# Optimization experiments

Measured on AMD Instinct MI355X. Metric: run time of the kernel, lower is better.

## Reference

```python
import jax, jax.numpy as jnp
import numpy as np

EMB = 1024

def setup_inputs() -> dict:
    key = jax.random.key(0)
    ks = jax.random.split(key, 7)
    s = 1.0 / np.sqrt(EMB)
    x = jax.random.normal(ks[0], (4, 2048, EMB), dtype=jnp.float32)
    Wk = jax.random.normal(ks[1], (EMB, EMB), dtype=jnp.float32) * s
    bk = jnp.zeros((EMB,), dtype=jnp.float32)
    Wq = jax.random.normal(ks[2], (EMB, EMB), dtype=jnp.float32) * s
    bq = jnp.zeros((EMB,), dtype=jnp.float32)
    Wv = jax.random.normal(ks[3], (EMB, EMB), dtype=jnp.float32) * s
    bv = jnp.zeros((EMB,), dtype=jnp.float32)
    return {"x": x, "Wk": Wk, "bk": bk, "Wq": Wq, "bq": bq, "Wv": Wv, "bv": bv}

def reference(x, Wk, bk, Wq, bq, Wv, bv):
    # Linear layers: x @ W.T + b (torch nn.Linear convention)
    k = jnp.einsum('bse,fe->bsf', x, Wk) + bk
    q = jnp.einsum('bse,fe->bsf', x, Wq) + bq
    v = jnp.einsum('bse,fe->bsf', x, Wv) + bv
    E = x.shape[-1]
    # NOTE: original computes k @ q^T (not q @ k^T) — reproduce faithfully.
    sim = jnp.einsum('bsd,btd->bst', k, q) / jnp.sqrt(jnp.float32(E))
    S = x.shape[1]
    causal = jnp.tril(jnp.ones((S, S), dtype=bool))  # [S,S]
    sim = jnp.where(causal, sim, -jnp.inf)
    attn = jax.nn.softmax(sim, axis=-1)
    return jnp.einsum('bst,btd->bsd', attn, v)
```

## Files before the change

### kernel.cpp

```cpp
#include <hip/hip_runtime.h>
#include <cstdint>


typedef __attribute__((ext_vector_type(8))) _Float16 f16x8;
typedef __attribute__((ext_vector_type(4))) float f32x4;

__device__ __forceinline__ unsigned short f2h(float x) {
  return __builtin_bit_cast(unsigned short, (_Float16)x);
}

__device__ __forceinline__ void lds_dma16(const void* g, void* l) {
  auto gp = reinterpret_cast<const __attribute__((address_space(1))) void*>(
      reinterpret_cast<uintptr_t>(g));
  auto lp = reinterpret_cast<__attribute__((address_space(3))) void*>(
      reinterpret_cast<uintptr_t>(l));
  __builtin_amdgcn_global_load_lds(gp, lp, 16, 0, 0);
}

__device__ __forceinline__ void gemm128(const unsigned short* __restrict__ Ag,
                                        const unsigned short* __restrict__ Bg,
                                        int lda, int ldb, int nk,
                                        unsigned short* As, unsigned short* Bs,
                                        f32x4 acc[4][4]) {
  const int tid = threadIdx.x;
  const int lane = tid & 63, wave = tid >> 6;
  const int wm = wave >> 1, wn = wave & 1;
  const int sr = lane >> 2;
  const int scb = (((lane & 3) ^ ((lane >> 3) & 3)) * 8);
  const int rr = lane & 15, qq = lane >> 4;
  const int slot = ((qq ^ ((rr >> 1) & 3)) * 8);

#pragma unroll
  for (int i = 0; i < 4; ++i)
#pragma unroll
    for (int j = 0; j < 4; ++j) {
      f32x4 z = {0.f, 0.f, 0.f, 0.f};
      acc[i][j] = z;
    }

#pragma unroll
  for (int c = 0; c < 2; ++c) {
    int chunk = wave * 2 + c;
    int row = chunk * 16 + sr;
    lds_dma16(Ag + (size_t)row * lda + scb, As + chunk * 512);
    lds_dma16(Bg + (size_t)row * ldb + scb, Bs + chunk * 512);
  }

  int buf = 0;
  for (int k0 = 0; k0 < nk; k0 += 32) {
    __syncthreads();
    const int kn = k0 + 32;
    if (kn < nk) {
      unsigned short* An = As + (buf ^ 1) * 4096;
      unsigned short* Bn = Bs + (buf ^ 1) * 4096;
#pragma unroll
      for (int c = 0; c < 2; ++c) {
        int chunk = wave * 2 + c;
        int row = chunk * 16 + sr;
        lds_dma16(Ag + (size_t)row * lda + kn + scb, An + chunk * 512);
        lds_dma16(Bg + (size_t)row * ldb + kn + scb, Bn + chunk * 512);
      }
    }

    f16x8 af[4], bf[4];
    const unsigned short* Ar = As + buf * 4096 + (wm * 64 + rr) * 32 + slot;
    const unsigned short* Br = Bs + buf * 4096 + (wn * 64 + rr) * 32 + slot;
#pragma unroll
    for (int i = 0; i < 4; ++i) af[i] = *(const f16x8*)(Ar + i * 512);
#pragma unroll
    for (int j = 0; j < 4; ++j) bf[j] = *(const f16x8*)(Br + j * 512);
#pragma unroll
    for (int i = 0; i < 4; ++i)
#pragma unroll
      for (int j = 0; j < 4; ++j)
        acc[i][j] = __builtin_amdgcn_mfma_f32_16x16x32_f16(af[i], bf[j],
                                                           acc[i][j], 0, 0, 0);
    buf ^= 1;
  }
}

__device__ __forceinline__ void gemm128_k64(
    const unsigned short* __restrict__ Ag, const unsigned short* __restrict__ Bg,
    int lda, int ldb, int nk, unsigned short* As, unsigned short* Bs,
    f32x4 acc[4][4]) {
  const int tid = threadIdx.x;
  const int lane = tid & 63, wave = tid >> 6;
  const int wm = wave >> 1, wn = wave & 1;
  const int sr = lane >> 3;
  const int scb = ((lane & 7) ^ sr) * 8;
  const int rr = lane & 15, qq = lane >> 4;
  const int slot0 = ((qq) ^ (rr & 7)) * 8;
  const int slot1 = ((4 + qq) ^ (rr & 7)) * 8;

#pragma unroll
  for (int i = 0; i < 4; ++i)
#pragma unroll
    for (int j = 0; j < 4; ++j) {
      f32x4 z = {0.f, 0.f, 0.f, 0.f};
      acc[i][j] = z;
    }

#pragma unroll
  for (int c = 0; c < 4; ++c) {
    int chunk = wave * 4 + c;
    int row = chunk * 8 + sr;
    lds_dma16(Ag + (size_t)row * lda + scb, As + chunk * 512);
    lds_dma16(Bg + (size_t)row * ldb + scb, Bs + chunk * 512);
  }

  int buf = 0;
  for (int k0 = 0; k0 < nk; k0 += 64) {
    __syncthreads();
    const int kn = k0 + 64;
    if (kn < nk) {
      unsigned short* An = As + (buf ^ 1) * 8192;
      unsigned short* Bn = Bs + (buf ^ 1) * 8192;
#pragma unroll
      for (int c = 0; c < 4; ++c) {
        int chunk = wave * 4 + c;
        int row = chunk * 8 + sr;
        lds_dma16(Ag + (size_t)row * lda + kn + scb, An + chunk * 512);
        lds_dma16(Bg + (size_t)row * ldb + kn + scb, Bn + chunk * 512);
      }
    }

    const unsigned short* Ar = As + buf * 8192 + (wm * 64 + rr) * 64;
    const unsigned short* Br = Bs + buf * 8192 + (wn * 64 + rr) * 64;
    {
      f16x8 af[4], bf[4];
#pragma unroll
      for (int i = 0; i < 4; ++i) af[i] = *(const f16x8*)(Ar + i * 1024 + slot0);
#pragma unroll
      for (int j = 0; j < 4; ++j) bf[j] = *(const f16x8*)(Br + j * 1024 + slot0);
#pragma unroll
      for (int i = 0; i < 4; ++i)
#pragma unroll
        for (int j = 0; j < 4; ++j)
          acc[i][j] = __builtin_amdgcn_mfma_f32_16x16x32_f16(af[i], bf[j],
                                                             acc[i][j], 0, 0, 0);
    }
    {
      f16x8 af[4], bf[4];
#pragma unroll
      for (int i = 0; i < 4; ++i) af[i] = *(const f16x8*)(Ar + i * 1024 + slot1);
#pragma unroll
      for (int j = 0; j < 4; ++j) bf[j] = *(const f16x8*)(Br + j * 1024 + slot1);
#pragma unroll
      for (int i = 0; i < 4; ++i)
#pragma unroll
        for (int j = 0; j < 4; ++j)
          acc[i][j] = __builtin_amdgcn_mfma_f32_16x16x32_f16(af[i], bf[j],
                                                             acc[i][j], 0, 0, 0);
    }
    buf ^= 1;
  }
}

__global__ void cvt_kernel(const float* __restrict__ x,
                           const float* __restrict__ w0,
                           const float* __restrict__ w1,
                           const float* __restrict__ w2,
                           unsigned short* __restrict__ dst,
                           float* __restrict__ rsum) {
  int i = blockIdx.x * 256 + threadIdx.x;
  if (i >= 2883584) {
    int z2 = i - 2883584;
    float4 z = {0.f, 0.f, 0.f, 0.f};
    ((float4*)rsum)[z2] = z;
    return;
  }
  const float* s;
  size_t si;
  if (i < 2097152) {
    s = x; si = i;
  } else {
    int j = i - 2097152;
    int z = j >> 18;
    s = (z == 0) ? w0 : ((z == 1) ? w1 : w2);
    si = j & 262143;
  }
  float4 f = ((const float4*)s)[si];
  ushort4 u;
  u.x = f2h(f.x); u.y = f2h(f.y); u.z = f2h(f.z); u.w = f2h(f.w);
  ((ushort4*)dst)[i] = u;
}

__global__ __launch_bounds__(256) void qkv_gemm_kernel(
    const unsigned short* __restrict__ xh, const unsigned short* __restrict__ wh,
    const float* __restrict__ bk, const float* __restrict__ bq,
    const float* __restrict__ bv, unsigned short* __restrict__ kh,
    unsigned short* __restrict__ qh, unsigned short* __restrict__ vT) {
  __shared__ unsigned short As[2 * 128 * 32], Bs[2 * 128 * 32];
  const int tn = blockIdx.x & 7, z = blockIdx.x >> 3;
  const unsigned short* W = wh + (size_t)z * 1048576;
  const int tm = blockIdx.y;

  const unsigned short* Ag = (z == 2) ? (W + (size_t)tn * 128 * 1024)
                                      : (xh + (size_t)tm * 128 * 1024);
  const unsigned short* Bg = (z == 2) ? (xh + (size_t)tm * 128 * 1024)
                                      : (W + (size_t)tn * 128 * 1024);

  f32x4 acc[4][4];
  gemm128(Ag, Bg, 1024, 1024, 1024, As, Bs, acc);

  const int lane = threadIdx.x & 63, wave = threadIdx.x >> 6;
  const int wm = wave >> 1, wn = wave & 1, rr = lane & 15, qq = lane >> 4;

  if (z == 2) {
#pragma unroll
    for (int i = 0; i < 4; ++i) {
      int d0 = tn * 128 + wm * 64 + i * 16 + qq * 4;
      float4 bi = *(const float4*)(bv + d0);
      float bir[4] = {bi.x, bi.y, bi.z, bi.w};
#pragma unroll
      for (int reg = 0; reg < 4; ++reg) {
        int d = d0 + reg;
#pragma unroll
        for (int j = 0; j < 4; ++j) {
          int tg = tm * 128 + wn * 64 + j * 16 + rr;
          int bb = tg >> 11, tt = tg & 2047;
          vT[((size_t)(bb * 1024 + d)) * 2048 + tt] =
              f2h(acc[i][j][reg] + bir[reg]);
        }
      }
    }
  } else {
    const float* bias = (z == 0) ? bk : bq;
    unsigned short* dst = (z == 0) ? kh : qh;
    float bj[4];
#pragma unroll
    for (int j = 0; j < 4; ++j)
      bj[j] = bias[tn * 128 + wn * 64 + j * 16 + rr];
#pragma unroll
    for (int i = 0; i < 4; ++i)
#pragma unroll
      for (int reg = 0; reg < 4; ++reg) {
        int gm = tm * 128 + wm * 64 + i * 16 + qq * 4 + reg;
#pragma unroll
        for (int j = 0; j < 4; ++j) {
          int gc = tn * 128 + wn * 64 + j * 16 + rr;
          dst[(size_t)gm * 1024 + gc] = f2h(acc[i][j][reg] + bj[j]);
        }
      }
  }
}

__global__ __launch_bounds__(256) void scores_kernel(
    const unsigned short* __restrict__ kh, const unsigned short* __restrict__ qh,
    unsigned short* __restrict__ P, float* __restrict__ rsum) {
  const int b = blockIdx.y;
  int idx = blockIdx.x;
  int ts = (int)((sqrtf(8.0f * idx + 1.0f) - 1.0f) * 0.5f);
  while ((ts + 1) * (ts + 2) / 2 <= idx) ++ts;
  while (ts * (ts + 1) / 2 > idx) --ts;
  const int tt = idx - ts * (ts + 1) / 2;
  __shared__ unsigned short As[2 * 128 * 64], Bs[2 * 128 * 64];

  f32x4 acc[4][4];
  gemm128_k64(kh + ((size_t)(b * 2048 + ts * 128)) * 1024,
              qh + ((size_t)(b * 2048 + tt * 128)) * 1024,
              1024, 1024, 1024, As, Bs, acc);

  const int lane = threadIdx.x & 63, wave = threadIdx.x >> 6;
  const int wm = wave >> 1, wn = wave & 1, rr = lane & 15, qq = lane >> 4;
  unsigned short* Pb = P + (size_t)b * 2048 * 2048;
  float* rs = rsum + b * 2048;
#pragma unroll
  for (int i = 0; i < 4; ++i)
#pragma unroll
    for (int reg = 0; reg < 4; ++reg) {
      int srow = ts * 128 + wm * 64 + i * 16 + qq * 4 + reg;
      float p = 0.f;
#pragma unroll
      for (int j = 0; j < 4; ++j) {
        int tcol = tt * 128 + wn * 64 + j * 16 + rr;
        float e = (tcol <= srow) ? __expf(acc[i][j][reg] * 0.03125f - 4.0f)
                                 : 0.0f;
        Pb[(size_t)srow * 2048 + tcol] = f2h(e);
        p += e;
      }
#pragma unroll
      for (int off = 1; off < 16; off <<= 1) p += __shfl_xor(p, off);
      if (rr == 0) atomicAdd(rs + srow, p);
    }
}

__global__ __launch_bounds__(256) void pv_gemm_kernel(
    const unsigned short* __restrict__ P, const unsigned short* __restrict__ vT,
    const float* __restrict__ rsum, float* __restrict__ out) {
  const int td = blockIdx.x, ts = 15 - blockIdx.y, b = blockIdx.z;
  __shared__ unsigned short As[2 * 128 * 64], Bs[2 * 128 * 64];

  f32x4 acc[4][4];
  gemm128_k64(P + ((size_t)(b * 2048 + ts * 128)) * 2048,
              vT + ((size_t)(b * 1024 + td * 128)) * 2048,
              2048, 2048, (ts + 1) * 128, As, Bs, acc);

  const int lane = threadIdx.x & 63, wave = threadIdx.x >> 6;
  const int wm = wave >> 1, wn = wave & 1, rr = lane & 15, qq = lane >> 4;
#pragma unroll
  for (int i = 0; i < 4; ++i) {
    int s0 = ts * 128 + wm * 64 + i * 16 + qq * 4;
    float4 r4 = *(const float4*)(rsum + b * 2048 + s0);
    float rv[4] = {__builtin_amdgcn_rcpf(r4.x), __builtin_amdgcn_rcpf(r4.y),
                   __builtin_amdgcn_rcpf(r4.z), __builtin_amdgcn_rcpf(r4.w)};
#pragma unroll
    for (int reg = 0; reg < 4; ++reg) {
      int srow = s0 + reg;
#pragma unroll
      for (int j = 0; j < 4; ++j) {
        int dcol = td * 128 + wn * 64 + j * 16 + rr;
        out[((size_t)(b * 2048 + srow)) * 1024 + dcol] =
            acc[i][j][reg] * rv[reg];
      }
    }
  }
}

extern "C" void kernel_launch(void* const* d_in, const int* in_sizes, int n_in,
                              void* d_out, int out_size, void* d_ws,
                              size_t ws_size, hipStream_t stream) {
  const float* x  = (const float*)d_in[0];
  const float* Wk = (const float*)d_in[1];
  const float* bk = (const float*)d_in[2];
  const float* Wq = (const float*)d_in[3];
  const float* bq = (const float*)d_in[4];
  const float* Wv = (const float*)d_in[5];
  const float* bv = (const float*)d_in[6];
  float* out = (float*)d_out;

  char* ws = (char*)d_ws;
  const size_t MB = 1ull << 20;
  unsigned short* xh = (unsigned short*)(ws + 0);
  unsigned short* wh = (unsigned short*)(ws + 16 * MB);
  unsigned short* P  = (unsigned short*)(ws + 0);
  unsigned short* kh = (unsigned short*)(ws + 38 * MB);
  unsigned short* qh = (unsigned short*)(ws + 54 * MB);
  unsigned short* vT = (unsigned short*)(ws + 70 * MB);
  float* rsum = (float*)(ws + 86 * MB);

  cvt_kernel<<<11272, 256, 0, stream>>>(x, Wk, Wq, Wv, xh, rsum);
  qkv_gemm_kernel<<<dim3(24, 64), 256, 0, stream>>>(xh, wh, bk, bq, bv,
                                                    kh, qh, vT);
  scores_kernel<<<dim3(136, 4), 256, 0, stream>>>(kh, qh, P, rsum);
  pv_gemm_kernel<<<dim3(8, 16, 4), 256, 0, stream>>>(P, vT, rsum, out);
}
```

Baseline: 239.7 us.

## Replace QKV projection GEMM with 256x256-tile, 8-wave pipelined kernel

The 128x128 QKV GEMM with K-step 32 is replaced by a 256x256 output tile per 512-thread block, using K-step 64 stages split into half-tiles. Staging is interleaved with the eight quadrant sub-iterations and controlled by explicit waitcnt, barriers and setprio, and the block-to-job mapping is remapped for L2 locality. The larger tile reuses each staged operand across more MMAs and cuts global traffic. In exchange it uses more LDS and registers per block, and the hand-tuned counter waits risk subtle races.

```diff
diff --git a/kernel.cpp b/kernel.cpp
--- a/kernel.cpp
+++ b/kernel.cpp
@@ -17,66 +17,113 @@
   __builtin_amdgcn_global_load_lds(gp, lp, 16, 0, 0);
 }
 
-__device__ __forceinline__ void gemm128(const unsigned short* __restrict__ Ag,
-                                        const unsigned short* __restrict__ Bg,
-                                        int lda, int ldb, int nk,
-                                        unsigned short* As, unsigned short* Bs,
-                                        f32x4 acc[4][4]) {
+__device__ __forceinline__ void stage_half(const unsigned short* __restrict__ G,
+                                           int ld, unsigned short* lds,
+                                           int tid) {
+  const int r = tid >> 3;
+  const int c = ((tid & 7) ^ (r & 7)) * 8;
+  lds_dma16(G + (size_t)r * ld + c, lds + tid * 8);
+  lds_dma16(G + (size_t)(r + 64) * ld + c, lds + 4096 + tid * 8);
+}
+
+__device__ __forceinline__ void g256_iter(
+    const unsigned short* __restrict__ Ag, const unsigned short* __restrict__ Bg,
+    int lda, int ldb, unsigned short* As, unsigned short* Bs,
+    f32x4 (&acc)[2][2][2][4], int k0, bool last) {
   const int tid = threadIdx.x;
   const int lane = tid & 63, wave = tid >> 6;
-  const int wm = wave >> 1, wn = wave & 1;
-  const int sr = lane >> 2;
-  const int scb = (((lane & 3) ^ ((lane >> 3) & 3)) * 8);
+  const int qwm = wave >> 1, qwn = wave & 1;
   const int rr = lane & 15, qq = lane >> 4;
-  const int slot = ((qq ^ ((rr >> 1) & 3)) * 8);
-
-#pragma unroll
-  for (int i = 0; i < 4; ++i)
-#pragma unroll
-    for (int j = 0; j < 4; ++j) {
-      f32x4 z = {0.f, 0.f, 0.f, 0.f};
-      acc[i][j] = z;
-    }
-
-#pragma unroll
-  for (int c = 0; c < 2; ++c) {
-    int chunk = wave * 2 + c;
-    int row = chunk * 16 + sr;
-    lds_dma16(Ag + (size_t)row * lda + scb, As + chunk * 512);
-    lds_dma16(Bg + (size_t)row * ldb + scb, Bs + chunk * 512);
-  }
-
-  int buf = 0;
-  for (int k0 = 0; k0 < nk; k0 += 32) {
-    __syncthreads();
-    const int kn = k0 + 32;
-    if (kn < nk) {
-      unsigned short* An = As + (buf ^ 1) * 4096;
-      unsigned short* Bn = Bs + (buf ^ 1) * 4096;
-#pragma unroll
-      for (int c = 0; c < 2; ++c) {
-        int chunk = wave * 2 + c;
-        int row = chunk * 16 + sr;
-        lds_dma16(Ag + (size_t)row * lda + kn + scb, An + chunk * 512);
-        lds_dma16(Bg + (size_t)row * ldb + kn + scb, Bn + chunk * 512);
+  const int arow = (qwm * 32 + rr) * 64;
+  const int brow = (qwn * 64 + rr) * 64;
+  const int s7 = rr & 7;
+  const int soff0 = (qq ^ s7) * 8;
+  const int soff1 = ((4 + qq) ^ s7) * 8;
+
+#pragma unroll
+  for (int p = 0; p < 8; ++p) {
+    const int buf = p >> 2, qm = (p >> 1) & 1, qn = p & 1;
+    const unsigned short* Ar = As + buf * 16384 + qm * 8192 + arow;
+    const unsigned short* Br = Bs + buf * 16384 + qn * 8192 + brow;
+    f16x8 af[2][2], bf[4][2];
+#pragma unroll
+    for (int fi = 0; fi < 2; ++fi) {
+      af[fi][0] = *(const f16x8*)(Ar + fi * 1024 + soff0);
+      af[fi][1] = *(const f16x8*)(Ar + fi * 1024 + soff1);
+    }
+#pragma unroll
+    for (int fj = 0; fj < 4; ++fj) {
+      bf[fj][0] = *(const f16x8*)(Br + fj * 1024 + soff0);
+      bf[fj][1] = *(const f16x8*)(Br + fj * 1024 + soff1);
+    }
+
+    if (p == 0) {
+      stage_half(Ag + (size_t)128 * lda + (k0 + 64), lda, As + 24576, tid);
+    } else if (p == 1) {
+      stage_half(Bg + (size_t)128 * ldb + (k0 + 64), ldb, Bs + 24576, tid);
+    } else if (!last) {
+      if (p == 2)      stage_half(Ag + (k0 + 128), lda, As, tid);
+      else if (p == 3) stage_half(Bg + (k0 + 128), ldb, Bs, tid);
+      else if (p == 4) stage_half(Ag + (size_t)128 * lda + (k0 + 128), lda, As + 8192, tid);
+      else if (p == 5) stage_half(Bg + (size_t)128 * ldb + (k0 + 128), ldb, Bs + 8192, tid);
+      else if (p == 6) stage_half(Ag + (k0 + 192), lda, As + 16384, tid);
+      else             stage_half(Bg + (k0 + 192), ldb, Bs + 16384, tid);
+    }
+
+    asm volatile("s_waitcnt lgkmcnt(8)" ::: "memory");
+    __builtin_amdgcn_s_barrier();
+    asm volatile("s_waitcnt lgkmcnt(0)" ::: "memory");
+    __builtin_amdgcn_sched_barrier(0);
+    __builtin_amdgcn_s_setprio(1);
+#pragma unroll
+    for (int h = 0; h < 2; ++h)
+#pragma unroll
+      for (int fi = 0; fi < 2; ++fi)
+#pragma unroll
+        for (int fj = 0; fj < 4; ++fj)
+          acc[qm][qn][fi][fj] = __builtin_amdgcn_mfma_f32_16x16x32_f16(
+              af[fi][h], bf[fj][h], acc[qm][qn][fi][fj], 0, 0, 0);
+    __builtin_amdgcn_s_setprio(0);
+    if (p == 3) {
+      if (last) asm volatile("s_waitcnt vmcnt(0)" ::: "memory");
+      else      asm volatile("s_waitcnt vmcnt(4)" ::: "memory");
+    } else if (p == 7 && !last) {
+      asm volatile("s_waitcnt vmcnt(4)" ::: "memory");
+    }
+    __builtin_amdgcn_s_barrier();
+  }
+}
+
+__device__ __forceinline__ void gemm256(
+    const unsigned short* __restrict__ Ag, const unsigned short* __restrict__ Bg,
+    int lda, int ldb, int nk, unsigned short* As, unsigned short* Bs,
+    f32x4 (&acc)[2][2][2][4]) {
+  const int tid = threadIdx.x;
+#pragma unroll
+  for (int a = 0; a < 2; ++a)
+#pragma unroll
+    for (int b = 0; b < 2; ++b)
+#pragma unroll
+      for (int c = 0; c < 2; ++c)
+#pragma unroll
+      for (int d = 0; d < 4; ++d) {
+        f32x4 z = {0.f, 0.f, 0.f, 0.f};
+        acc[a][b][c][d] = z;
       }
-    }
-
-    f16x8 af[4], bf[4];
-    const unsigned short* Ar = As + buf * 4096 + (wm * 64 + rr) * 32 + slot;
-    const unsigned short* Br = Bs + buf * 4096 + (wn * 64 + rr) * 32 + slot;
-#pragma unroll
-    for (int i = 0; i < 4; ++i) af[i] = *(const f16x8*)(Ar + i * 512);
-#pragma unroll
-    for (int j = 0; j < 4; ++j) bf[j] = *(const f16x8*)(Br + j * 512);
-#pragma unroll
-    for (int i = 0; i < 4; ++i)
-#pragma unroll
-      for (int j = 0; j < 4; ++j)
-        acc[i][j] = __builtin_amdgcn_mfma_f32_16x16x32_f16(af[i], bf[j],
-                                                           acc[i][j], 0, 0, 0);
-    buf ^= 1;
-  }
+
+  stage_half(Ag, lda, As, tid);
+  stage_half(Ag + (size_t)128 * lda, lda, As + 8192, tid);
+  stage_half(Bg, ldb, Bs, tid);
+  stage_half(Bg + (size_t)128 * ldb, ldb, Bs + 8192, tid);
+  stage_half(Ag + 64, lda, As + 16384, tid);
+  stage_half(Bg + 64, ldb, Bs + 16384, tid);
+  asm volatile("s_waitcnt vmcnt(4)" ::: "memory");
+  __builtin_amdgcn_s_barrier();
+
+  const int NIT = nk >> 7;
+  for (int it = 0; it < NIT - 1; ++it)
+    g256_iter(Ag, Bg, lda, ldb, As, Bs, acc, it << 7, false);
+  g256_iter(Ag, Bg, lda, ldb, As, Bs, acc, (NIT - 1) << 7, true);
 }
 
 __device__ __forceinline__ void gemm128_k64(
@@ -185,61 +232,84 @@
   ((ushort4*)dst)[i] = u;
 }
 
-__global__ __launch_bounds__(256) void qkv_gemm_kernel(
+__global__ __launch_bounds__(512, 2) void qkv256_kernel(
     const unsigned short* __restrict__ xh, const unsigned short* __restrict__ wh,
     const float* __restrict__ bk, const float* __restrict__ bq,
     const float* __restrict__ bv, unsigned short* __restrict__ kh,
     unsigned short* __restrict__ qh, unsigned short* __restrict__ vT) {
-  __shared__ unsigned short As[2 * 128 * 32], Bs[2 * 128 * 32];
-  const int tn = blockIdx.x & 7, z = blockIdx.x >> 3;
-  const unsigned short* W = wh + (size_t)z * 1048576;
-  const int tm = blockIdx.y;
-
-  const unsigned short* Ag = (z == 2) ? (W + (size_t)tn * 128 * 1024)
-                                      : (xh + (size_t)tm * 128 * 1024);
-  const unsigned short* Bg = (z == 2) ? (xh + (size_t)tm * 128 * 1024)
-                                      : (W + (size_t)tn * 128 * 1024);
-
-  f32x4 acc[4][4];
-  gemm128(Ag, Bg, 1024, 1024, 1024, As, Bs, acc);
-
-  const int lane = threadIdx.x & 63, wave = threadIdx.x >> 6;
-  const int wm = wave >> 1, wn = wave & 1, rr = lane & 15, qq = lane >> 4;
-
-  if (z == 2) {
-#pragma unroll
-    for (int i = 0; i < 4; ++i) {
-      int d0 = tn * 128 + wm * 64 + i * 16 + qq * 4;
-      float4 bi = *(const float4*)(bv + d0);
-      float bir[4] = {bi.x, bi.y, bi.z, bi.w};
-#pragma unroll
-      for (int reg = 0; reg < 4; ++reg) {
-        int d = d0 + reg;
-#pragma unroll
-        for (int j = 0; j < 4; ++j) {
-          int tg = tm * 128 + wn * 64 + j * 16 + rr;
-          int bb = tg >> 11, tt = tg & 2047;
-          vT[((size_t)(bb * 1024 + d)) * 2048 + tt] =
-              f2h(acc[i][j][reg] + bir[reg]);
+  __shared__ unsigned short As[32768], Bs[32768];
+  const int job = (blockIdx.x & 7) * 48 + (blockIdx.x >> 3);
+
+  const unsigned short* Ag;
+  const unsigned short* Bg;
+  if (job < 256) {
+    const int tm = job >> 3, tn = job & 7;
+    Ag = xh + (size_t)tm * 256 * 1024;
+    Bg = wh + (size_t)tn * 256 * 1024;
+  } else {
+    const int j = job - 256;
+    const int dt = j >> 5, tt = j & 31;
+    Ag = wh + 2097152 + (size_t)dt * 256 * 1024;
+    Bg = xh + (size_t)tt * 256 * 1024;
+  }
+
+  f32x4 acc[2][2][2][4];
+  gemm256(Ag, Bg, 1024, 1024, 1024, As, Bs, acc);
+
+  const int tid = threadIdx.x;
+  const int lane = tid & 63, wave = tid >> 6;
+  const int qwm = wave >> 1, qwn = wave & 1, rr = lane & 15, qq = lane >> 4;
+
+  if (job < 256) {
+    const int tm = job >> 3, tn = job & 7;
+    const bool isq = tn >= 4;
+    unsigned short* dst = isq ? qh : kh;
+    const float* bias = isq ? bq : bk;
+    const int nbase = (tn & 3) * 256;
+    float bj[2][4];
+#pragma unroll
+    for (int qn = 0; qn < 2; ++qn)
+#pragma unroll
+      for (int fj = 0; fj < 4; ++fj)
+        bj[qn][fj] = bias[nbase + qn * 128 + qwn * 64 + fj * 16 + rr];
+#pragma unroll
+    for (int qm = 0; qm < 2; ++qm)
+#pragma unroll
+      for (int fi = 0; fi < 2; ++fi)
+#pragma unroll
+        for (int reg = 0; reg < 4; ++reg) {
+          const int m = tm * 256 + qm * 128 + qwm * 32 + fi * 16 + qq * 4 + reg;
+#pragma unroll
+          for (int qn = 0; qn < 2; ++qn)
+#pragma unroll
+            for (int fj = 0; fj < 4; ++fj) {
+              const int n = nbase + qn * 128 + qwn * 64 + fj * 16 + rr;
+              dst[(size_t)m * 1024 + n] =
+                  f2h(acc[qm][qn][fi][fj][reg] + bj[qn][fj]);
+            }
         }
-      }
-    }
   } else {
-    const float* bias = (z == 0) ? bk : bq;
-    unsigned short* dst = (z == 0) ? kh : qh;
-    float bj[4];
-#pragma unroll
-    for (int j = 0; j < 4; ++j)
-      bj[j] = bias[tn * 128 + wn * 64 + j * 16 + rr];
-#pragma unroll
-    for (int i = 0; i < 4; ++i)
-#pragma unroll
-      for (int reg = 0; reg < 4; ++reg) {
-        int gm = tm * 128 + wm * 64 + i * 16 + qq * 4 + reg;
-#pragma unroll
-        for (int j = 0; j < 4; ++j) {
-          int gc = tn * 128 + wn * 64 + j * 16 + rr;
-          dst[(size_t)gm * 1024 + gc] = f2h(acc[i][j][reg] + bj[j]);
+    const int j = job - 256;
+    const int dt = j >> 5, tt = j & 31;
+#pragma unroll
+    for (int qm = 0; qm < 2; ++qm)
+#pragma unroll
+      for (int fi = 0; fi < 2; ++fi) {
+        const int d0 = dt * 256 + qm * 128 + qwm * 32 + fi * 16 + qq * 4;
+        const float4 b4 = *(const float4*)(bv + d0);
+        const float bir[4] = {b4.x, b4.y, b4.z, b4.w};
+#pragma unroll
+        for (int reg = 0; reg < 4; ++reg) {
+          const int d = d0 + reg;
+#pragma unroll
+          for (int qn = 0; qn < 2; ++qn)
+#pragma unroll
+            for (int fj = 0; fj < 4; ++fj) {
+              const int tg = tt * 256 + qn * 128 + qwn * 64 + fj * 16 + rr;
+              const int bb = tg >> 11, t = tg & 2047;
+              vT[((size_t)(bb * 1024 + d)) * 2048 + t] =
+                  f2h(acc[qm][qn][fi][fj][reg] + bir[reg]);
+            }
         }
       }
   }
@@ -340,8 +410,7 @@
   float* rsum = (float*)(ws + 86 * MB);
 
   cvt_kernel<<<11272, 256, 0, stream>>>(x, Wk, Wq, Wv, xh, rsum);
-  qkv_gemm_kernel<<<dim3(24, 64), 256, 0, stream>>>(xh, wh, bk, bq, bv,
-                                                    kh, qh, vT);
+  qkv256_kernel<<<384, 512, 0, stream>>>(xh, wh, bk, bq, bv, kh, qh, vT);
   scores_kernel<<<dim3(136, 4), 256, 0, stream>>>(kh, qh, P, rsum);
   pv_gemm_kernel<<<dim3(8, 16, 4), 256, 0, stream>>>(P, vT, rsum, out);
 }
```

Result: slower. 244.7 us (+2.1%).

## Use atomic work-queue tile scheduling for scores and PV kernels

Applied to the files above, without the earlier changes.

The scores and PV GEMM kernels now run a fixed grid of 512 blocks that pull tile indices from global atomic counters, instead of mapping one block per tile. The counters are reset in the conversion kernel. PV tiles are dispatched in descending causal-length order across all batches, so the longest K-loops start first. This aims to cut tail imbalance on triangular work, at the cost of an extra atomic and a block-wide barrier per tile.

```diff
diff --git a/kernel.cpp b/kernel.cpp
--- a/kernel.cpp
+++ b/kernel.cpp
@@ -79,6 +79,7 @@
   }
 }
 
+
 __device__ __forceinline__ void gemm128_k64(
     const unsigned short* __restrict__ Ag, const unsigned short* __restrict__ Bg,
     int lda, int ldb, int nk, unsigned short* As, unsigned short* Bs,
@@ -161,12 +162,13 @@
                            const float* __restrict__ w1,
                            const float* __restrict__ w2,
                            unsigned short* __restrict__ dst,
-                           float* __restrict__ rsum) {
+                           float* __restrict__ rsum, int* __restrict__ cnt) {
   int i = blockIdx.x * 256 + threadIdx.x;
   if (i >= 2883584) {
     int z2 = i - 2883584;
     float4 z = {0.f, 0.f, 0.f, 0.f};
     ((float4*)rsum)[z2] = z;
+    if (z2 == 0) { cnt[0] = 0; cnt[1] = 0; }
     return;
   }
   const float* s;
@@ -247,71 +249,93 @@
 
 __global__ __launch_bounds__(256) void scores_kernel(
     const unsigned short* __restrict__ kh, const unsigned short* __restrict__ qh,
-    unsigned short* __restrict__ P, float* __restrict__ rsum) {
-  const int b = blockIdx.y;
-  int idx = blockIdx.x;
-  int ts = (int)((sqrtf(8.0f * idx + 1.0f) - 1.0f) * 0.5f);
-  while ((ts + 1) * (ts + 2) / 2 <= idx) ++ts;
-  while (ts * (ts + 1) / 2 > idx) --ts;
-  const int tt = idx - ts * (ts + 1) / 2;
+    unsigned short* __restrict__ P, float* __restrict__ rsum,
+    int* __restrict__ cnt) {
   __shared__ unsigned short As[2 * 128 * 64], Bs[2 * 128 * 64];
-
-  f32x4 acc[4][4];
-  gemm128_k64(kh + ((size_t)(b * 2048 + ts * 128)) * 1024,
-              qh + ((size_t)(b * 2048 + tt * 128)) * 1024,
-              1024, 1024, 1024, As, Bs, acc);
-
-  const int lane = threadIdx.x & 63, wave = threadIdx.x >> 6;
-  const int wm = wave >> 1, wn = wave & 1, rr = lane & 15, qq = lane >> 4;
-  unsigned short* Pb = P + (size_t)b * 2048 * 2048;
-  float* rs = rsum + b * 2048;
-#pragma unroll
-  for (int i = 0; i < 4; ++i)
-#pragma unroll
-    for (int reg = 0; reg < 4; ++reg) {
-      int srow = ts * 128 + wm * 64 + i * 16 + qq * 4 + reg;
-      float p = 0.f;
-#pragma unroll
-      for (int j = 0; j < 4; ++j) {
-        int tcol = tt * 128 + wn * 64 + j * 16 + rr;
-        float e = (tcol <= srow) ? __expf(acc[i][j][reg] * 0.03125f - 4.0f)
-                                 : 0.0f;
-        Pb[(size_t)srow * 2048 + tcol] = f2h(e);
-        p += e;
-      }
-#pragma unroll
-      for (int off = 1; off < 16; off <<= 1) p += __shfl_xor(p, off);
-      if (rr == 0) atomicAdd(rs + srow, p);
-    }
+  __shared__ int js;
+  const int tid = threadIdx.x;
+
+  for (;;) {
+    if (tid == 0) js = atomicAdd(cnt, 1);
+    __syncthreads();
+    const int j = js;
+    if (j >= 544) return;
+
+    const int b = j / 136;
+    int idx = j - b * 136;
+    int ts = (int)((sqrtf(8.0f * idx + 1.0f) - 1.0f) * 0.5f);
+    while ((ts + 1) * (ts + 2) / 2 <= idx) ++ts;
+    while (ts * (ts + 1) / 2 > idx) --ts;
+    const int tt = idx - ts * (ts + 1) / 2;
+
+    f32x4 acc[4][4];
+    gemm128_k64(kh + ((size_t)(b * 2048 + ts * 128)) * 1024,
+                qh + ((size_t)(b * 2048 + tt * 128)) * 1024,
+                1024, 1024, 1024, As, Bs, acc);
+
+    const int lane = tid & 63, wave = tid >> 6;
+    const int wm = wave >> 1, wn = wave & 1, rr = lane & 15, qq = lane >> 4;
+    unsigned short* Pb = P + (size_t)b * 2048 * 2048;
+    float* rs = rsum + b * 2048;
+#pragma unroll
+    for (int i = 0; i < 4; ++i)
+#pragma unroll
+      for (int reg = 0; reg < 4; ++reg) {
+        int srow = ts * 128 + wm * 64 + i * 16 + qq * 4 + reg;
+        float p = 0.f;
+#pragma unroll
+        for (int jj = 0; jj < 4; ++jj) {
+          int tcol = tt * 128 + wn * 64 + jj * 16 + rr;
+          float e = (tcol <= srow) ? __expf(acc[i][jj][reg] * 0.03125f - 4.0f)
+                                   : 0.0f;
+          Pb[(size_t)srow * 2048 + tcol] = f2h(e);
+          p += e;
+        }
+#pragma unroll
+        for (int off = 1; off < 16; off <<= 1) p += __shfl_xor(p, off);
+        if (rr == 0) atomicAdd(rs + srow, p);
+      }
+  }
 }
 
 __global__ __launch_bounds__(256) void pv_gemm_kernel(
     const unsigned short* __restrict__ P, const unsigned short* __restrict__ vT,
-    const float* __restrict__ rsum, float* __restrict__ out) {
-  const int td = blockIdx.x, ts = 15 - blockIdx.y, b = blockIdx.z;
+    const float* __restrict__ rsum, float* __restrict__ out,
+    int* __restrict__ cnt) {
   __shared__ unsigned short As[2 * 128 * 64], Bs[2 * 128 * 64];
-
-  f32x4 acc[4][4];
-  gemm128_k64(P + ((size_t)(b * 2048 + ts * 128)) * 2048,
-              vT + ((size_t)(b * 1024 + td * 128)) * 2048,
-              2048, 2048, (ts + 1) * 128, As, Bs, acc);
-
-  const int lane = threadIdx.x & 63, wave = threadIdx.x >> 6;
-  const int wm = wave >> 1, wn = wave & 1, rr = lane & 15, qq = lane >> 4;
-#pragma unroll
-  for (int i = 0; i < 4; ++i) {
-    int s0 = ts * 128 + wm * 64 + i * 16 + qq * 4;
-    float4 r4 = *(const float4*)(rsum + b * 2048 + s0);
-    float rv[4] = {__builtin_amdgcn_rcpf(r4.x), __builtin_amdgcn_rcpf(r4.y),
-                   __builtin_amdgcn_rcpf(r4.z), __builtin_amdgcn_rcpf(r4.w)};
-#pragma unroll
-    for (int reg = 0; reg < 4; ++reg) {
-      int srow = s0 + reg;
-#pragma unroll
-      for (int j = 0; j < 4; ++j) {
-        int dcol = td * 128 + wn * 64 + j * 16 + rr;
-        out[((size_t)(b * 2048 + srow)) * 1024 + dcol] =
-            acc[i][j][reg] * rv[reg];
+  __shared__ int js;
+  const int tid = threadIdx.x;
+
+  for (;;) {
+    if (tid == 0) js = atomicAdd(cnt + 1, 1);
+    __syncthreads();
+    const int j = js;
+    if (j >= 512) return;
+
+    const int ts = 15 - (j >> 5), b = (j >> 3) & 3, td = j & 7;
+
+    f32x4 acc[4][4];
+    gemm128_k64(P + ((size_t)(b * 2048 + ts * 128)) * 2048,
+                vT + ((size_t)(b * 1024 + td * 128)) * 2048,
+                2048, 2048, (ts + 1) * 128, As, Bs, acc);
+
+    const int lane = tid & 63, wave = tid >> 6;
+    const int wm = wave >> 1, wn = wave & 1, rr = lane & 15, qq = lane >> 4;
+#pragma unroll
+    for (int i = 0; i < 4; ++i) {
+      int s0 = ts * 128 + wm * 64 + i * 16 + qq * 4;
+      float4 r4 = *(const float4*)(rsum + b * 2048 + s0);
+      float rv[4] = {__builtin_amdgcn_rcpf(r4.x), __builtin_amdgcn_rcpf(r4.y),
+                     __builtin_amdgcn_rcpf(r4.z), __builtin_amdgcn_rcpf(r4.w)};
+#pragma unroll
+      for (int reg = 0; reg < 4; ++reg) {
+        int srow = s0 + reg;
+#pragma unroll
+        for (int jj = 0; jj < 4; ++jj) {
+          int dcol = td * 128 + wn * 64 + jj * 16 + rr;
+          out[((size_t)(b * 2048 + srow)) * 1024 + dcol] =
+              acc[i][jj][reg] * rv[reg];
+        }
       }
     }
   }
@@ -334,14 +358,15 @@
   unsigned short* xh = (unsigned short*)(ws + 0);
   unsigned short* wh = (unsigned short*)(ws + 16 * MB);
   unsigned short* P  = (unsigned short*)(ws + 0);
+  int* cnt = (int*)(ws + 36 * MB);
   unsigned short* kh = (unsigned short*)(ws + 38 * MB);
   unsigned short* qh = (unsigned short*)(ws + 54 * MB);
   unsigned short* vT = (unsigned short*)(ws + 70 * MB);
   float* rsum = (float*)(ws + 86 * MB);
 
-  cvt_kernel<<<11272, 256, 0, stream>>>(x, Wk, Wq, Wv, xh, rsum);
+  cvt_kernel<<<11272, 256, 0, stream>>>(x, Wk, Wq, Wv, xh, rsum, cnt);
   qkv_gemm_kernel<<<dim3(24, 64), 256, 0, stream>>>(xh, wh, bk, bq, bv,
                                                     kh, qh, vT);
-  scores_kernel<<<dim3(136, 4), 256, 0, stream>>>(kh, qh, P, rsum);
-  pv_gemm_kernel<<<dim3(8, 16, 4), 256, 0, stream>>>(P, vT, rsum, out);
-}
+  scores_kernel<<<512, 256, 0, stream>>>(kh, qh, P, rsum, cnt);
+  pv_gemm_kernel<<<512, 256, 0, stream>>>(P, vT, rsum, out, cnt);
+}
```

New measurement: 241.9 us. Within noise of the previous version (+0.9%).

## Split-K PV GEMM with persistent atomic work queue and K32 tiles

Applied to the files above, without the earlier changes.

Drops the K64 GEMM helper and uses the K32 gemm128 for both scores and PV. PV becomes a persistent kernel that pulls jobs from an atomic counter, splits each causal row tile's K range into 512-wide chunks, and accumulates results into out with float atomics. cvt_kernel now zeroes out and the counters. The aim is to balance the triangular PV workload across CUs, at the cost of atomic output traffic, extra zeroing, and nondeterministic summation order.

```diff
diff --git a/kernel.cpp b/kernel.cpp
--- a/kernel.cpp
+++ b/kernel.cpp
@@ -79,94 +79,25 @@
   }
 }
 
-__device__ __forceinline__ void gemm128_k64(
-    const unsigned short* __restrict__ Ag, const unsigned short* __restrict__ Bg,
-    int lda, int ldb, int nk, unsigned short* As, unsigned short* Bs,
-    f32x4 acc[4][4]) {
-  const int tid = threadIdx.x;
-  const int lane = tid & 63, wave = tid >> 6;
-  const int wm = wave >> 1, wn = wave & 1;
-  const int sr = lane >> 3;
-  const int scb = ((lane & 7) ^ sr) * 8;
-  const int rr = lane & 15, qq = lane >> 4;
-  const int slot0 = ((qq) ^ (rr & 7)) * 8;
-  const int slot1 = ((4 + qq) ^ (rr & 7)) * 8;
-
-#pragma unroll
-  for (int i = 0; i < 4; ++i)
-#pragma unroll
-    for (int j = 0; j < 4; ++j) {
-      f32x4 z = {0.f, 0.f, 0.f, 0.f};
-      acc[i][j] = z;
-    }
-
-#pragma unroll
-  for (int c = 0; c < 4; ++c) {
-    int chunk = wave * 4 + c;
-    int row = chunk * 8 + sr;
-    lds_dma16(Ag + (size_t)row * lda + scb, As + chunk * 512);
-    lds_dma16(Bg + (size_t)row * ldb + scb, Bs + chunk * 512);
-  }
-
-  int buf = 0;
-  for (int k0 = 0; k0 < nk; k0 += 64) {
-    __syncthreads();
-    const int kn = k0 + 64;
-    if (kn < nk) {
-      unsigned short* An = As + (buf ^ 1) * 8192;
-      unsigned short* Bn = Bs + (buf ^ 1) * 8192;
-#pragma unroll
-      for (int c = 0; c < 4; ++c) {
-        int chunk = wave * 4 + c;
-        int row = chunk * 8 + sr;
-        lds_dma16(Ag + (size_t)row * lda + kn + scb, An + chunk * 512);
-        lds_dma16(Bg + (size_t)row * ldb + kn + scb, Bn + chunk * 512);
-      }
-    }
-
-    const unsigned short* Ar = As + buf * 8192 + (wm * 64 + rr) * 64;
-    const unsigned short* Br = Bs + buf * 8192 + (wn * 64 + rr) * 64;
-    {
-      f16x8 af[4], bf[4];
-#pragma unroll
-      for (int i = 0; i < 4; ++i) af[i] = *(const f16x8*)(Ar + i * 1024 + slot0);
-#pragma unroll
-      for (int j = 0; j < 4; ++j) bf[j] = *(const f16x8*)(Br + j * 1024 + slot0);
-#pragma unroll
-      for (int i = 0; i < 4; ++i)
-#pragma unroll
-        for (int j = 0; j < 4; ++j)
-          acc[i][j] = __builtin_amdgcn_mfma_f32_16x16x32_f16(af[i], bf[j],
-                                                             acc[i][j], 0, 0, 0);
-    }
-    {
-      f16x8 af[4], bf[4];
-#pragma unroll
-      for (int i = 0; i < 4; ++i) af[i] = *(const f16x8*)(Ar + i * 1024 + slot1);
-#pragma unroll
-      for (int j = 0; j < 4; ++j) bf[j] = *(const f16x8*)(Br + j * 1024 + slot1);
-#pragma unroll
-      for (int i = 0; i < 4; ++i)
-#pragma unroll
-        for (int j = 0; j < 4; ++j)
-          acc[i][j] = __builtin_amdgcn_mfma_f32_16x16x32_f16(af[i], bf[j],
-                                                             acc[i][j], 0, 0, 0);
-    }
-    buf ^= 1;
-  }
-}
-
 __global__ void cvt_kernel(const float* __restrict__ x,
                            const float* __restrict__ w0,
                            const float* __restrict__ w1,
                            const float* __restrict__ w2,
                            unsigned short* __restrict__ dst,
-                           float* __restrict__ rsum) {
+                           float* __restrict__ rsum, int* __restrict__ cnt,
+                           float* __restrict__ out) {
   int i = blockIdx.x * 256 + threadIdx.x;
+  if (i >= 2885632) {
+    int o = i - 2885632;
+    float4 z = {0.f, 0.f, 0.f, 0.f};
+    ((float4*)out)[o] = z;
+    return;
+  }
   if (i >= 2883584) {
     int z2 = i - 2883584;
     float4 z = {0.f, 0.f, 0.f, 0.f};
     ((float4*)rsum)[z2] = z;
+    if (z2 == 0) { cnt[0] = 0; cnt[1] = 0; }
     return;
   }
   const float* s;
@@ -254,12 +185,12 @@
   while ((ts + 1) * (ts + 2) / 2 <= idx) ++ts;
   while (ts * (ts + 1) / 2 > idx) --ts;
   const int tt = idx - ts * (ts + 1) / 2;
-  __shared__ unsigned short As[2 * 128 * 64], Bs[2 * 128 * 64];
+  __shared__ unsigned short As[2 * 128 * 32], Bs[2 * 128 * 32];
 
   f32x4 acc[4][4];
-  gemm128_k64(kh + ((size_t)(b * 2048 + ts * 128)) * 1024,
-              qh + ((size_t)(b * 2048 + tt * 128)) * 1024,
-              1024, 1024, 1024, As, Bs, acc);
+  gemm128(kh + ((size_t)(b * 2048 + ts * 128)) * 1024,
+          qh + ((size_t)(b * 2048 + tt * 128)) * 1024,
+          1024, 1024, 1024, As, Bs, acc);
 
   const int lane = threadIdx.x & 63, wave = threadIdx.x >> 6;
   const int wm = wave >> 1, wn = wave & 1, rr = lane & 15, qq = lane >> 4;
@@ -287,31 +218,57 @@
 
 __global__ __launch_bounds__(256) void pv_gemm_kernel(
     const unsigned short* __restrict__ P, const unsigned short* __restrict__ vT,
-    const float* __restrict__ rsum, float* __restrict__ out) {
-  const int td = blockIdx.x, ts = 15 - blockIdx.y, b = blockIdx.z;
-  __shared__ unsigned short As[2 * 128 * 64], Bs[2 * 128 * 64];
-
-  f32x4 acc[4][4];
-  gemm128_k64(P + ((size_t)(b * 2048 + ts * 128)) * 2048,
-              vT + ((size_t)(b * 1024 + td * 128)) * 2048,
-              2048, 2048, (ts + 1) * 128, As, Bs, acc);
-
-  const int lane = threadIdx.x & 63, wave = threadIdx.x >> 6;
-  const int wm = wave >> 1, wn = wave & 1, rr = lane & 15, qq = lane >> 4;
-#pragma unroll
-  for (int i = 0; i < 4; ++i) {
-    int s0 = ts * 128 + wm * 64 + i * 16 + qq * 4;
-    float4 r4 = *(const float4*)(rsum + b * 2048 + s0);
-    float rv[4] = {__builtin_amdgcn_rcpf(r4.x), __builtin_amdgcn_rcpf(r4.y),
-                   __builtin_amdgcn_rcpf(r4.z), __builtin_amdgcn_rcpf(r4.w)};
-#pragma unroll
-    for (int reg = 0; reg < 4; ++reg) {
-      int srow = s0 + reg;
-#pragma unroll
-      for (int j = 0; j < 4; ++j) {
-        int dcol = td * 128 + wn * 64 + j * 16 + rr;
-        out[((size_t)(b * 2048 + srow)) * 1024 + dcol] =
-            acc[i][j][reg] * rv[reg];
+    const float* __restrict__ rsum, float* __restrict__ out,
+    int* __restrict__ cnt) {
+  __shared__ unsigned short As[2 * 128 * 32], Bs[2 * 128 * 32];
+  __shared__ int js;
+  const int tid = threadIdx.x;
+
+  for (;;) {
+    if (tid == 0) js = atomicAdd(cnt + 1, 1);
+    __syncthreads();
+    const int j = js;
+    if (j >= 1280) return;
+
+    int ts, b, td, kc;
+    if (j < 512) {
+      ts = 15 - (j >> 7); int r = j & 127;
+      b = r >> 5; td = (r >> 2) & 7; kc = r & 3;
+    } else if (j < 896) {
+      int q = j - 512; ts = 11 - q / 96; int r = q % 96;
+      b = r / 24; int r2 = r % 24; td = r2 / 3; kc = r2 % 3;
+    } else if (j < 1152) {
+      int q = j - 896; ts = 7 - (q >> 6); int r = q & 63;
+      b = r >> 4; td = (r >> 1) & 7; kc = r & 1;
+    } else {
+      int q = j - 1152; ts = 3 - (q >> 5); int r = q & 31;
+      b = r >> 3; td = r & 7; kc = 0;
+    }
+    const int kbeg = kc * 512;
+    const int nk = min(512, (ts + 1) * 128 - kbeg);
+
+    f32x4 acc[4][4];
+    gemm128(P + ((size_t)(b * 2048 + ts * 128)) * 2048 + kbeg,
+            vT + ((size_t)(b * 1024 + td * 128)) * 2048 + kbeg,
+            2048, 2048, nk, As, Bs, acc);
+
+    const int lane = tid & 63, wave = tid >> 6;
+    const int wm = wave >> 1, wn = wave & 1, rr = lane & 15, qq = lane >> 4;
+#pragma unroll
+    for (int i = 0; i < 4; ++i) {
+      int s0 = ts * 128 + wm * 64 + i * 16 + qq * 4;
+      float4 r4 = *(const float4*)(rsum + b * 2048 + s0);
+      float rv[4] = {__builtin_amdgcn_rcpf(r4.x), __builtin_amdgcn_rcpf(r4.y),
+                     __builtin_amdgcn_rcpf(r4.z), __builtin_amdgcn_rcpf(r4.w)};
+#pragma unroll
+      for (int reg = 0; reg < 4; ++reg) {
+        int srow = s0 + reg;
+#pragma unroll
+        for (int jj = 0; jj < 4; ++jj) {
+          int dcol = td * 128 + wn * 64 + jj * 16 + rr;
+          atomicAdd(&out[((size_t)(b * 2048 + srow)) * 1024 + dcol],
+                    acc[i][jj][reg] * rv[reg]);
+        }
       }
     }
   }
@@ -334,14 +291,15 @@
   unsigned short* xh = (unsigned short*)(ws + 0);
   unsigned short* wh = (unsigned short*)(ws + 16 * MB);
   unsigned short* P  = (unsigned short*)(ws + 0);
+  int* cnt = (int*)(ws + 36 * MB);
   unsigned short* kh = (unsigned short*)(ws + 38 * MB);
   unsigned short* qh = (unsigned short*)(ws + 54 * MB);
   unsigned short* vT = (unsigned short*)(ws + 70 * MB);
   float* rsum = (float*)(ws + 86 * MB);
 
-  cvt_kernel<<<11272, 256, 0, stream>>>(x, Wk, Wq, Wv, xh, rsum);
+  cvt_kernel<<<19464, 256, 0, stream>>>(x, Wk, Wq, Wv, xh, rsum, cnt, out);
   qkv_gemm_kernel<<<dim3(24, 64), 256, 0, stream>>>(xh, wh, bk, bq, bv,
                                                     kh, qh, vT);
   scores_kernel<<<dim3(136, 4), 256, 0, stream>>>(kh, qh, P, rsum);
-  pv_gemm_kernel<<<dim3(8, 16, 4), 256, 0, stream>>>(P, vT, rsum, out);
-}
+  pv_gemm_kernel<<<1024, 256, 0, stream>>>(P, vT, rsum, out, cnt);
+}
```

Measured after the change: 299.9 us. 25.2% more time.
